# Kernel tuning notes

Measured on AMD Instinct MI355X. Metric: run time of the kernel, lower is better.

Reference implementation:

```python
import jax, jax.numpy as jnp
import numpy as np

R = 3          # radius
T_STEPS = 2    # T
F = 200        # fingerprint_dim
AOUT = 39
BOUT = 10
B, L, N, NB = 128, 256, 8, 512


def _gru(x, h, wih, whh, bih, bhh):
    # PyTorch GRUCell semantics; wih/whh: [3F, F], gate order r,z,n
    gi = x @ wih.T + bih
    gh = h @ whh.T + bhh
    ir, iz, inn = jnp.split(gi, 3, axis=-1)
    hr, hz, hn = jnp.split(gh, 3, axis=-1)
    r = jax.nn.sigmoid(ir + hr)
    z = jax.nn.sigmoid(iz + hz)
    n = jnp.tanh(inn + r * hn)
    return (1.0 - z) * n + z * h


def _seg_softmax(x, lo, hi):
    idx = jnp.arange(x.shape[-1])
    m = ((idx >= lo) & (idx < hi)).astype(x.dtype)
    s = jax.nn.softmax(x + (1.0 - m) * (-9e8), axis=-1)
    return s * m


def _unit_act(x, i, fn):
    m = (jnp.arange(x.shape[-1]) == i).astype(x.dtype)
    return fn(x * m) * m


def setup_inputs() -> dict:
    key = jax.random.key(0)
    ks = jax.random.split(key, 24)
    rn = lambda k, s, sc=0.05: (jax.random.normal(k, s, jnp.float32) * sc)
    inp = {
        'atom_list': rn(ks[0], (B, L, AOUT), 1.0),
        'bond_list': rn(ks[1], (B, NB, BOUT), 1.0),
        'atom_degree_list': jax.random.randint(ks[2], (B, L, N), 0, L),
        'bond_degree_list': jax.random.randint(ks[3], (B, L, N), 0, NB),
        'atom_mask': jnp.ones((B, L), jnp.float32),
        'mol_feature': rn(ks[4], (B, F), 1.0),
        'activated_features': jax.nn.relu(rn(ks[5], (B, L, F), 1.0)),
        # params
        'atom_fc_w': rn(ks[6], (AOUT, F)), 'atom_fc_b': jnp.zeros((AOUT,), jnp.float32),
        'bond_fc_w': rn(ks[7], (BOUT, 2 * F)), 'bond_fc_b': jnp.zeros((BOUT,), jnp.float32),
        'align_w': rn(ks[8], (R, F, 2 * F)), 'align_b': jnp.zeros((R, F), jnp.float32),
        'attend_w': rn(ks[9], (R, F, F)), 'attend_b': jnp.zeros((R, F), jnp.float32),
        'gru_wih': rn(ks[10], (R, 3 * F, F)), 'gru_whh': rn(ks[11], (R, 3 * F, F)),
        'gru_bih': jnp.zeros((R, 3 * F), jnp.float32), 'gru_bhh': jnp.zeros((R, 3 * F), jnp.float32),
        'mol_align_w': rn(ks[12], (F, 2 * F)), 'mol_align_b': jnp.zeros((F,), jnp.float32),
        'mol_gru_wih': rn(ks[13], (3 * F, F)), 'mol_gru_whh': rn(ks[14], (3 * F, F)),
        'mol_gru_bih': jnp.zeros((3 * F,), jnp.float32), 'mol_gru_bhh': jnp.zeros((3 * F,), jnp.float32),
    }
    return inp


def reference(atom_list, bond_list, atom_degree_list, bond_degree_list, atom_mask,
              mol_feature, activated_features,
              atom_fc_w, atom_fc_b, bond_fc_w, bond_fc_b,
              align_w, align_b, attend_w, attend_b,
              gru_wih, gru_whh, gru_bih, gru_bhh,
              mol_align_w, mol_align_b,
              mol_gru_wih, mol_gru_whh, mol_gru_bih, mol_gru_bhh):
    f32 = jnp.float32
    b, l, _ = atom_list.shape
    fdim = mol_feature.shape[-1]
    gather = jax.vmap(lambda feats, idx: feats[idx])  # [L,F],[L,N] -> [L,N,F]

    pad = (atom_degree_list == l - 1)
    attend_mask = jnp.where(pad, 0.0, 1.0).astype(f32)[..., None]      # [B,L,N,1]
    softmax_mask = jnp.where(pad, -9e8, 0.0).astype(f32)[..., None]    # [B,L,N,1]

    # molecular feature -> per-atom git feature (T GRU steps)
    mol_exp = jnp.broadcast_to(mol_feature[:, None, :], (b, l, fdim))
    mw = jax.nn.softmax(jnp.sum(mol_exp * activated_features, axis=-1), axis=-1)  # [B,L]
    git = mw[..., None] * mol_exp + activated_features
    for _t in range(T_STEPS):
        ctx = jax.nn.elu(jnp.concatenate([mol_exp, git], axis=-1) @ mol_align_w.T + mol_align_b)
        git = _gru(ctx.reshape(b * l, fdim), git.reshape(b * l, fdim),
                   mol_gru_wih, mol_gru_whh, mol_gru_bih, mol_gru_bhh).reshape(b, l, fdim)
        act = jax.nn.relu(git)

    # radius-1 rounds of neighbor attention + GRU update
    for d in range(R - 1):
        nbr = gather(act, atom_degree_list)                             # [B,L,N,F]
        exp = jnp.broadcast_to(act[:, :, None, :], nbr.shape)
        feat_align = jnp.concatenate([exp, nbr], axis=-1)               # [B,L,N,2F]
        score = jax.nn.leaky_relu(feat_align @ align_w[d].T + align_b[d], 0.01)
        score = score + softmax_mask
        attw = jax.nn.softmax(score, axis=-2) * attend_mask             # [B,L,N,F]
        nt = nbr @ attend_w[d].T + attend_b[d]
        context = jax.nn.elu(jnp.sum(attw * nt, axis=-2))               # [B,L,F]
        h = _gru(context.reshape(b * l, fdim), act.reshape(b * l, fdim),
                 gru_wih[d], gru_whh[d], gru_bih[d], gru_bhh[d])
        act = jax.nn.relu(h.reshape(b, l, fdim))

    # decode atoms and bonds
    al = act @ atom_fc_w.T + atom_fc_b                                  # [B,L,AOUT]
    nbr = gather(act, atom_degree_list)                                 # [B,L,N,F]
    exp = jnp.broadcast_to(act[:, :, None, :], nbr.shape)
    bl = jnp.concatenate([exp, nbr], axis=-1) @ bond_fc_w.T + bond_fc_b  # [B,L,N,BOUT]

    sig = jax.nn.sigmoid
    activate_atom = (_seg_softmax(al, 0, 16) + _seg_softmax(al, 16, 22)
                     + _seg_softmax(al, 24, 30) + _seg_softmax(al, 31, 36)
                     + _unit_act(al, 24, jax.nn.relu)
                     + _unit_act(al, 30, sig) + _unit_act(al, 36, sig)
                     + _unit_act(al, 37, sig) + _unit_act(al, 38, sig))
    activate_bond = (_seg_softmax(bl, 0, 4) + _seg_softmax(bl, 6, 10)
                     + _unit_act(bl, 4, sig) + _unit_act(bl, 5, sig))
    return (activate_atom, activate_bond)
```

## Files before the change

### kernel.cpp

```cpp
#include <hip/hip_runtime.h>
#include <hip/hip_bf16.h>

#define FDIM 200
#define BB   128
#define LL   256
#define NN   8
#define BL   (BB*LL)
#define AOUTD 39
#define BOUTD 10
#define KCH  28

#define P0 0
#define P1 17920
#define P2 25088
#define P3 46592
#define P4 82432
#define P5 103936
#define P6 139776
#define P7 161280
#define WCHUNKS 164864
#define NBIAS 4864

typedef short v8s __attribute__((ext_vector_type(8)));
typedef float v4f __attribute__((ext_vector_type(4)));

__device__ __forceinline__ float bf2f(unsigned short u){
  union { unsigned int i; float f; } v; v.i = ((unsigned int)u) << 16; return v.f;
}
__device__ __forceinline__ unsigned short f2bf(float f){
  unsigned int x = __float_as_uint(f);
  x += 0x7fffu + ((x >> 16) & 1u);
  return (unsigned short)(x >> 16);
}
__device__ __forceinline__ float ldf(const void* p, long long i, bool bf){
  return bf ? bf2f(((const unsigned short*)p)[i]) : ((const float*)p)[i];
}
__device__ __forceinline__ void stf(void* p, size_t i, float v, bool bf){
  if (bf) ((unsigned short*)p)[i] = f2bf(v);
  else    ((float*)p)[i] = v;
}
__device__ __forceinline__ float bflo(unsigned int q){
  union { unsigned int i; float f; } v; v.i = q << 16; return v.f;
}
__device__ __forceinline__ float bfhi(unsigned int q){
  union { unsigned int i; float f; } v; v.i = q & 0xffff0000u; return v.f;
}
__device__ __forceinline__ void ld8(const unsigned short* p, float* o){
  uint4 q = *(const uint4*)p;
  o[0]=bflo(q.x); o[1]=bfhi(q.x); o[2]=bflo(q.y); o[3]=bfhi(q.y);
  o[4]=bflo(q.z); o[5]=bfhi(q.z); o[6]=bflo(q.w); o[7]=bfhi(q.w);
}
__device__ __forceinline__ void ld8g(const void* p, size_t i, bool bf, float* o){
  if (bf){ ld8((const unsigned short*)p + i, o); }
  else {
    const float4* q = (const float4*)((const float*)p + i);
    float4 x = q[0], y = q[1];
    o[0]=x.x; o[1]=x.y; o[2]=x.z; o[3]=x.w;
    o[4]=y.x; o[5]=y.y; o[6]=y.z; o[7]=y.w;
  }
}
__device__ __forceinline__ void st8(unsigned short* p, const float* v){
  uint4 q;
  q.x = (unsigned int)f2bf(v[0]) | ((unsigned int)f2bf(v[1]) << 16);
  q.y = (unsigned int)f2bf(v[2]) | ((unsigned int)f2bf(v[3]) << 16);
  q.z = (unsigned int)f2bf(v[4]) | ((unsigned int)f2bf(v[5]) << 16);
  q.w = (unsigned int)f2bf(v[6]) | ((unsigned int)f2bf(v[7]) << 16);
  *(uint4*)p = q;
}
__device__ __forceinline__ float dotF(const void* wp, size_t off, const float* x, bool bf){
  float a0=0.f,a1=0.f,a2=0.f,a3=0.f;
  if (bf){
    const uint4* p = (const uint4*)((const unsigned short*)wp + off);
#pragma unroll
    for (int c = 0; c < FDIM/8; ++c){
      uint4 q = p[c];
      const float* xb = x + c*8;
      a0 += bflo(q.x)*xb[0]; a1 += bfhi(q.x)*xb[1];
      a2 += bflo(q.y)*xb[2]; a3 += bfhi(q.y)*xb[3];
      a0 += bflo(q.z)*xb[4]; a1 += bfhi(q.z)*xb[5];
      a2 += bflo(q.w)*xb[6]; a3 += bfhi(q.w)*xb[7];
    }
  } else {
    const float4* p = (const float4*)((const float*)wp + off);
#pragma unroll
    for (int c = 0; c < FDIM/4; ++c){
      float4 q = p[c];
      const float* xb = x + c*4;
      a0 += q.x*xb[0]; a1 += q.y*xb[1]; a2 += q.z*xb[2]; a3 += q.w*xb[3];
    }
  }
  return (a0+a1)+(a2+a3);
}
__device__ __forceinline__ float sigm(float x){ return 1.f/(1.f+__expf(-x)); }
__device__ __forceinline__ float tanh_(float x){
  float cx = fminf(fmaxf(x, -15.f), 15.f);
  float e = __expf(2.f*cx);
  return (e - 1.f)/(e + 1.f);
}
__device__ __forceinline__ float elu_(float x){ return x > 0.f ? x : __expf(x) - 1.f; }

__global__ void k_probe(const unsigned int* __restrict__ amask, int* __restrict__ mode){
  if (blockIdx.x == 0 && threadIdx.x == 0)
    *mode = (amask[0] == 0x3F803F80u) ? 1 : 0;
}

__global__ __launch_bounds__(256) void k_repack(unsigned short* __restrict__ wrep,
    const void* mwhh, const void* maw, const void* mwih,
    const void* alw, const void* atw, const void* gwhh, const void* gwih,
    const void* afw, const void* bfw, const int* __restrict__ mode){
  const bool bf = (*mode != 0);
  int idx = blockIdx.x*256 + threadIdx.x;
  if (idx >= WCHUNKS) return;
  int pb, Ng, pad = 0; long long d = 0;
  if (idx < P1)      { pb = P0; Ng = 640;  }
  else if (idx < P2) { pb = P1; Ng = 256;  }
  else if (idx < P3) { pb = P2; Ng = 768;  pad = 1; }
  else if (idx < P4) { pb = P3; Ng = 1280; }
  else if (idx < P5) { pb = P4; Ng = 768;  pad = 1; }
  else if (idx < P6) { pb = P5; Ng = 1280; d = 1; }
  else if (idx < P7) { pb = P6; Ng = 768;  pad = 1; d = 1; }
  else               { pb = P7; Ng = 128;  }
  int li = idx - pb;
  int c = li / Ng, n = li - c*Ng;
  const void* S = nullptr; long long sb = 0; int rl = 0, off = 0, row = 0, N = 0;
  if (pad){
    int gate = n >> 8, f = n & 255;
    if (f < 200){
      S = (pb == P2) ? mwih : gwih;
      sb = (pb == P2) ? 0 : d*120000;
      rl = 200; off = 0; row = gate*200 + f; N = Ng;
    }
  }
  else if (pb == P0)      { S = mwhh; rl = 200; row = n; N = 600; }
  else if (pb == P1) { S = maw;  rl = 400; off = 200; row = n; N = 200; }
  else if (pb == P3 || pb == P5){
    N = 1200;
    if (n < 200)      { S = alw;  sb = d*80000;  rl = 400; off = 0;   row = n; }
    else if (n < 400) { S = alw;  sb = d*80000;  rl = 400; off = 200; row = n-200; }
    else if (n < 600) { S = atw;  sb = d*40000;  rl = 200; off = 0;   row = n-400; }
    else              { S = gwhh; sb = d*120000; rl = 200; off = 0;   row = n-600; }
  } else {
    N = 64;
    if (n < 39)                { S = afw; rl = 200; row = n; }
    else if (n >= 40 && n < 50){ S = bfw; rl = 400; off = 0;   row = n-40; }
    else if (n >= 50 && n < 60){ S = bfw; rl = 400; off = 200; row = n-50; }
  }
  float v[8];
#pragma unroll
  for (int j = 0; j < 8; j++){
    int k = c*8 + j;
    v[j] = (S && n < N && k < 200) ? ldf(S, sb + (long long)row*rl + off + k, bf) : 0.f;
  }
  st8(wrep + (size_t)idx*8, v);
}

__global__ __launch_bounds__(256) void k_biases(float* __restrict__ bt,
    const void* mbhh, const void* mbih, const void* alb, const void* atb,
    const void* gbhh, const void* gbih, const void* afb, const void* bfb,
    const int* __restrict__ mode){
  const bool bf = (*mode != 0);
  int e = blockIdx.x*256 + threadIdx.x;
  if (e >= NBIAS) return;
  float v = 0.f;
  if (e < 600)        v = ldf(mbhh, e, bf);
  else if (e < 1200)  v = ldf(mbih, e-600, bf);
  else if (e < 4800){
    int q = e - 1200; int d = q / 1800; q -= d*1800;
    if (q < 1200){
      if (q < 200)      v = ldf(alb, (long long)d*200 + q, bf);
      else if (q < 400) v = 0.f;
      else if (q < 600) v = ldf(atb, (long long)d*200 + q-400, bf);
      else              v = ldf(gbhh, (long long)d*600 + q-600, bf);
    } else              v = ldf(gbih, (long long)d*600 + q-1200, bf);
  } else {
    int q = e - 4800;
    if (q < 39)                 v = ldf(afb, q, bf);
    else if (q >= 40 && q < 50) v = ldf(bfb, q-40, bf);
  }
  bt[e] = v;
}

__global__ __launch_bounds__(256, 5) void k_gemm(
    const unsigned short* __restrict__ A,
    const unsigned short* __restrict__ Wc, int wNg, int npan,
    unsigned short* __restrict__ C, int ldc, int Nout,
    int emode, const float* __restrict__ bias, int gbase)
{
  __shared__ unsigned short Ws[KCH*64*8];
  int t = threadIdx.x;
  int bid = blockIdx.x;
  int res = bid & 7, q = bid >> 3;
  int p = q % npan;
  int mt = (q / npan)*8 + res;
  int nbase = p * 64;
  int mbase = mt * 128;
  const uint4* Wg = (const uint4*)Wc;
  uint4* Wl = (uint4*)Ws;
  for (int i = t; i < KCH*64; i += 256){
    int c = i >> 6, n = i & 63;
    Wl[i] = Wg[(size_t)c*wNg + nbase + n];
  }
  __syncthreads();
  int wave = t >> 6, lane = t & 63;
  int quad = lane >> 4, l16 = lane & 15;
  const unsigned short* A0 = A + (size_t)(mbase + wave*32 + l16)*FDIM + quad*8;
  v4f acc[2][4];
#pragma unroll
  for (int ms = 0; ms < 2; ms++)
#pragma unroll
    for (int ns = 0; ns < 4; ns++) acc[ms][ns] = (v4f){0.f,0.f,0.f,0.f};
#pragma unroll
  for (int ks = 0; ks < 7; ks++){
    v8s a0 = *(const v8s*)(A0 + ks*32);
    v8s a1 = *(const v8s*)(A0 + 16*FDIM + ks*32);
    const unsigned short* Bp = Ws + ((ks*4 + quad)*64 + l16)*8;
#pragma unroll
    for (int ns = 0; ns < 4; ns++){
      v8s b = *(const v8s*)(Bp + ns*128);
      acc[0][ns] = __builtin_amdgcn_mfma_f32_16x16x32_bf16(a0, b, acc[0][ns], 0, 0, 0);
      acc[1][ns] = __builtin_amdgcn_mfma_f32_16x16x32_bf16(a1, b, acc[1][ns], 0, 0, 0);
    }
  }
  __syncthreads();
  const float* pr = (emode == 2) ? (bias + (size_t)(((gbase + mbase) >> 8))*FDIM) : nullptr;
#pragma unroll
  for (int ms = 0; ms < 2; ms++){
#pragma unroll
    for (int ns = 0; ns < 4; ns++){
      int lcol = l16 + ns*16;
      int col = nbase + lcol;
      float badd = (emode == 1) ? bias[col] : 0.f;
      float pv   = (emode == 2) ? pr[col] : 0.f;
      int lrow = wave*32 + ms*16 + quad*4;
#pragma unroll
      for (int reg = 0; reg < 4; reg++){
        float v = acc[ms][ns][reg] + badd;
        if (emode == 2) v = elu_(pv + v);
        Ws[(lrow + reg)*72 + lcol] = f2bf(v);
      }
    }
  }
  __syncthreads();
#pragma unroll
  for (int j = 0; j < 4; j++){
    int g = t + j*256;
    int row = g >> 3, cg = g & 7;
    int col = nbase + cg*8;
    if (col < Nout){
      uint4 qv = *(const uint4*)(Ws + row*72 + cg*8);
      *(uint4*)(C + (size_t)(mbase + row)*ldc + col) = qv;
    }
  }
}

__global__ __launch_bounds__(256, 3) void k_gemm_gru(
    const unsigned short* __restrict__ ctxA,
    const unsigned short* __restrict__ Wc,
    unsigned short* __restrict__ act,
    const unsigned short* __restrict__ big, int gho,
    const float* __restrict__ gib, int dorelu)
{
  __shared__ unsigned short Ws[3*KCH*32*8];
  int t = threadIdx.x, bid = blockIdx.x;
  int res = bid & 7, q = bid >> 3;
  int p = q % 7;
  int mt = (q / 7)*8 + res;
  int f0 = p*32;
  int mbase = mt*128;
  const uint4* Wg = (const uint4*)Wc;
  uint4* Wl = (uint4*)Ws;
  for (int i = t; i < 3*KCH*32; i += 256){
    int g = i / (KCH*32), r2 = i - g*(KCH*32);
    int c = r2 >> 5, n = r2 & 31;
    Wl[i] = Wg[(size_t)c*768 + g*256 + f0 + n];
  }
  __syncthreads();
  int wave = t >> 6, lane = t & 63;
  int quad = lane >> 4, l16 = lane & 15;
  const unsigned short* A0 = ctxA + (size_t)(mbase + wave*32 + l16)*FDIM + quad*8;
  v4f acc[3][2][2];
#pragma unroll
  for (int g = 0; g < 3; g++)
#pragma unroll
    for (int ms = 0; ms < 2; ms++)
#pragma unroll
      for (int ns = 0; ns < 2; ns++) acc[g][ms][ns] = (v4f){0.f,0.f,0.f,0.f};
#pragma unroll
  for (int ks = 0; ks < 7; ks++){
    v8s a0 = *(const v8s*)(A0 + ks*32);
    v8s a1 = *(const v8s*)(A0 + 16*FDIM + ks*32);
#pragma unroll
    for (int g = 0; g < 3; g++){
      const unsigned short* Bp = Ws + ((size_t)(g*KCH + ks*4 + quad)*32 + l16)*8;
#pragma unroll
      for (int ns = 0; ns < 2; ns++){
        v8s b = *(const v8s*)(Bp + ns*128);
        acc[g][0][ns] = __builtin_amdgcn_mfma_f32_16x16x32_bf16(a0, b, acc[g][0][ns], 0, 0, 0);
        acc[g][1][ns] = __builtin_amdgcn_mfma_f32_16x16x32_bf16(a1, b, acc[g][1][ns], 0, 0, 0);
      }
    }
  }
  int rowb = mbase + wave*32 + quad*4;
#pragma unroll
  for (int ms = 0; ms < 2; ms++){
#pragma unroll
    for (int ns = 0; ns < 2; ns++){
      int f = f0 + ns*16 + l16;
      if (f < 200){
        float br = gib[f], bz = gib[200+f], bn = gib[400+f];
#pragma unroll
        for (int reg = 0; reg < 4; reg++){
          int row = rowb + ms*16 + reg;
          size_t gb = (size_t)row*1200 + gho;
          float ghr = bf2f(big[gb + f]);
          float ghz = bf2f(big[gb + 200 + f]);
          float ghn = bf2f(big[gb + 400 + f]);
          float h = bf2f(act[(size_t)row*FDIM + f]);
          float r = sigm(acc[0][ms][ns][reg] + br + ghr);
          float z = sigm(acc[1][ms][ns][reg] + bz + ghz);
          float n = tanh_(acc[2][ms][ns][reg] + bn + r*ghn);
          float hn = (1.f - z)*n + z*h;
          if (dorelu) hn = fmaxf(hn, 0.f);
          act[(size_t)row*FDIM + f] = f2bf(hn);
        }
      }
    }
  }
}

__global__ __launch_bounds__(256) void k_premol(float* __restrict__ pre,
    const void* __restrict__ molf, const void* __restrict__ maw,
    const void* __restrict__ mab, const int* __restrict__ mode){
  const bool bf = (*mode != 0);
  int b = blockIdx.x, t = threadIdx.x;
  __shared__ float mf[FDIM];
  for (int f = t; f < FDIM; f += 256) mf[f] = ldf(molf, (size_t)b*FDIM+f, bf);
  __syncthreads();
  for (int f = t; f < FDIM; f += 256)
    pre[b*FDIM+f] = ldf(mab, f, bf) + dotF(maw, (size_t)f*2*FDIM, mf, bf);
}

__global__ __launch_bounds__(LL) void k_gitdot(float* __restrict__ mw_out,
    const void* __restrict__ molf, const void* __restrict__ actf,
    const int* __restrict__ mode){
  const bool bf = (*mode != 0);
  int b = blockIdx.x, l = threadIdx.x;
  __shared__ float mf[FDIM];
  __shared__ float red[LL];
  for (int f = l; f < FDIM; f += LL) mf[f] = ldf(molf, (size_t)b*FDIM+f, bf);
  __syncthreads();
  float d = dotF(actf, ((size_t)b*LL + l)*FDIM, mf, bf);
  red[l] = d; __syncthreads();
  for (int s = 128; s > 0; s >>= 1){ if (l < s) red[l] = fmaxf(red[l], red[l+s]); __syncthreads(); }
  float m = red[0]; __syncthreads();
  float e = __expf(d - m);
  red[l] = e; __syncthreads();
  for (int s = 128; s > 0; s >>= 1){ if (l < s) red[l] += red[l+s]; __syncthreads(); }
  mw_out[(size_t)b*LL + l] = e / red[0];
}

__global__ __launch_bounds__(256) void k_gitwrite(unsigned short* __restrict__ act,
    const void* __restrict__ molf, const void* __restrict__ actf,
    const float* __restrict__ mw, const int* __restrict__ mode){
  const bool bf = (*mode != 0);
  int idx = blockIdx.x*256 + threadIdx.x;
  if (idx >= BL*25) return;
  int row = idx/25, f0 = (idx - row*25)*8;
  int b = row >> 8;
  float m = mw[row];
  float mv[8], av[8], v[8];
  ld8g(molf, (size_t)b*FDIM + f0, bf, mv);
  ld8g(actf, (size_t)row*FDIM + f0, bf, av);
#pragma unroll
  for (int j = 0; j < 8; j++) v[j] = m*mv[j] + av[j];
  st8(act + (size_t)row*FDIM + f0, v);
}

__global__ __launch_bounds__(256) void k_attn_ew(const unsigned short* __restrict__ big,
    unsigned short* __restrict__ ctx, const int* __restrict__ adeg,
    int base, int total){
  int idx = blockIdx.x*256 + threadIdx.x;
  if (idx >= total) return;
  int a = idx/25, f0 = (idx - a*25)*8;
  int mb = (a >> 8) << 8;
  float s0[8];
  ld8(big + (size_t)a*1200 + f0, s0);
  int4 d0 = *(const int4*)(adeg + (size_t)(base + a)*NN);
  int4 d1 = *(const int4*)(adeg + (size_t)(base + a)*NN + 4);
  int iv[NN] = {d0.x, d0.y, d0.z, d0.w, d1.x, d1.y, d1.z, d1.w};
  int nid[NN]; float nmul[NN], nadd[NN];
#pragma unroll
  for (int n = 0; n < NN; n++){
    nid[n] = mb + iv[n];
    bool pad = (iv[n] == LL-1);
    nmul[n] = pad ? 0.f : 1.f;
    nadd[n] = pad ? -9e8f : 0.f;
  }
  float e[NN][8], mx[8];
#pragma unroll
  for (int j = 0; j < 8; j++) mx[j] = -1e30f;
#pragma unroll
  for (int n = 0; n < NN; n++){
    float p[8];
    ld8(big + (size_t)nid[n]*1200 + 200 + f0, p);
#pragma unroll
    for (int j = 0; j < 8; j++){
      float s = s0[j] + p[j];
      s = s > 0.f ? s : 0.01f*s;
      s += nadd[n];
      e[n][j] = s;
      mx[j] = fmaxf(mx[j], s);
    }
  }
  float sum[8] = {0,0,0,0,0,0,0,0};
#pragma unroll
  for (int n = 0; n < NN; n++)
#pragma unroll
    for (int j = 0; j < 8; j++){ e[n][j] = __expf(e[n][j] - mx[j]); sum[j] += e[n][j]; }
  float acc[8] = {0,0,0,0,0,0,0,0};
#pragma unroll
  for (int n = 0; n < NN; n++){
    float q[8];
    ld8(big + (size_t)nid[n]*1200 + 400 + f0, q);
#pragma unroll
    for (int j = 0; j < 8; j++) acc[j] += e[n][j]*nmul[n]*q[j];
  }
  float o[8];
#pragma unroll
  for (int j = 0; j < 8; j++) o[j] = elu_(acc[j]/sum[j]);
  st8(ctx + (size_t)a*FDIM + f0, o);
}

__global__ __launch_bounds__(256) void k_dec(const unsigned short* __restrict__ big,
    const int* __restrict__ adeg, void* __restrict__ out, int base,
    const int* __restrict__ mode){
  const bool bf = (*mode != 0);
  const size_t obase = (size_t)BL*AOUTD;
  int sub = threadIdx.x >> 6, tl = threadIdx.x & 63;
  int a = blockIdx.x*4 + sub;
  __shared__ float al[4][40];
  __shared__ float sm[4][4], ss[4][4];
  const int lo[4] = {0,16,24,31}, hi[4] = {16,22,30,36};
  if (tl < AOUTD) al[sub][tl] = bf2f(big[(size_t)a*64 + tl]);
  __syncthreads();
  if (tl < 4){
    float m = -1e30f;
    for (int k = lo[tl]; k < hi[tl]; k++) m = fmaxf(m, al[sub][k]);
    float s = 0.f;
    for (int k = lo[tl]; k < hi[tl]; k++) s += __expf(al[sub][k]-m);
    sm[sub][tl] = m; ss[sub][tl] = s;
  }
  __syncthreads();
  if (tl < AOUTD){
    float v = 0.f;
#pragma unroll
    for (int g = 0; g < 4; g++)
      if (tl >= lo[g] && tl < hi[g]) v += __expf(al[sub][tl]-sm[sub][g])/ss[sub][g];
    if (tl == 24) v += fmaxf(al[sub][24], 0.f);
    if (tl == 30 || tl == 36 || tl == 37 || tl == 38) v += sigm(al[sub][tl]);
    stf(out, (size_t)(base + a)*AOUTD + tl, v, bf);
  } else if (tl >= 40 && tl < 48){
    int n = tl - 40;
    int iv = adeg[((size_t)(base + a))*NN + n];
    int vr = ((a >> 8) << 8) + iv;
    float bl[BOUTD];
#pragma unroll
    for (int o = 0; o < BOUTD; o++)
      bl[o] = bf2f(big[(size_t)a*64 + 40 + o]) + bf2f(big[(size_t)vr*64 + 50 + o]);
    float v[BOUTD];
    float m0 = fmaxf(fmaxf(bl[0],bl[1]), fmaxf(bl[2],bl[3]));
    float e0[4], s0 = 0.f;
#pragma unroll
    for (int j = 0; j < 4; j++){ e0[j] = __expf(bl[j]-m0); s0 += e0[j]; }
    float m1 = fmaxf(fmaxf(bl[6],bl[7]), fmaxf(bl[8],bl[9]));
    float e1[4], s1 = 0.f;
#pragma unroll
    for (int j = 0; j < 4; j++){ e1[j] = __expf(bl[6+j]-m1); s1 += e1[j]; }
#pragma unroll
    for (int j = 0; j < 4; j++) v[j] = e0[j]/s0;
    v[4] = sigm(bl[4]); v[5] = sigm(bl[5]);
#pragma unroll
    for (int j = 0; j < 4; j++) v[6+j] = e1[j]/s1;
    size_t op = obase + ((size_t)(base + a)*NN + n)*BOUTD;
#pragma unroll
    for (int j = 0; j < BOUTD; j++) stf(out, op + j, v[j], bf);
  }
}

extern "C" void kernel_launch(void* const* d_in, const int* in_sizes, int n_in,
                              void* d_out, int out_size, void* d_ws, size_t ws_size,
                              hipStream_t stream) {
  const int* adeg = (const int*)d_in[2];
  const void* amask = d_in[4];
  const void* molf = d_in[5];
  const void* actf = d_in[6];
  const void* afw = d_in[7];  const void* afb = d_in[8];
  const void* bfw = d_in[9];  const void* bfb = d_in[10];
  const void* alw = d_in[11]; const void* alb = d_in[12];
  const void* atw = d_in[13]; const void* atb = d_in[14];
  const void* gwih = d_in[15]; const void* gwhh = d_in[16];
  const void* gbih = d_in[17]; const void* gbhh = d_in[18];
  const void* maw = d_in[19]; const void* mab = d_in[20];
  const void* mwih = d_in[21]; const void* mwhh = d_in[22];
  const void* mbih = d_in[23]; const void* mbhh = d_in[24];

  char* w = (char*)d_ws;
  unsigned short* act  = (unsigned short*)w;  w += (size_t)BL*FDIM*2;
  float*          mw   = (float*)w;           w += (size_t)BL*4;
  float*          pre  = (float*)w;           w += (size_t)BB*FDIM*4;
  unsigned short* wrep = (unsigned short*)w;  w += (size_t)WCHUNKS*16;
  float*          bt   = (float*)w;           w += (size_t)NBIAS*4;
  int*            mode = (int*)w;             w += 16;
  size_t fixed = (size_t)(w - (char*)d_ws);
  int CH = 8192;
  if (ws_size >= fixed + (size_t)32768*2800) CH = 32768;
  else if (ws_size >= fixed + (size_t)16384*2800) CH = 16384;
  unsigned short* ctx = (unsigned short*)w;   w += (size_t)CH*FDIM*2;
  unsigned short* big = (unsigned short*)w;
  const int NCH = BL / CH;
  const int EWT = CH*25, EWB = EWT/256;
  const int GY = CH/128;

  k_probe<<<1, 64, 0, stream>>>((const unsigned int*)amask, mode);
  k_repack<<<(WCHUNKS + 255)/256, 256, 0, stream>>>(wrep, mwhh, maw, mwih,
      alw, atw, gwhh, gwih, afw, bfw, mode);
  k_biases<<<(NBIAS + 255)/256, 256, 0, stream>>>(bt, mbhh, mbih, alb, atb,
      gbhh, gbih, afb, bfb, mode);
  k_premol<<<BB, 256, 0, stream>>>(pre, molf, maw, mab, mode);
  k_gitdot<<<BB, LL, 0, stream>>>(mw, molf, actf, mode);
  k_gitwrite<<<(BL*25 + 255)/256, 256, 0, stream>>>(act, molf, actf, mw, mode);

  for (int ts = 0; ts < 2; ts++){
    for (int c = 0; c < NCH; c++){
      int base = c*CH;
      unsigned short* Ac = act + (size_t)base*FDIM;
      k_gemm<<<10*GY, 256, 0, stream>>>(Ac, wrep + (size_t)P0*8, 640, 10,
          big, 1200, 600, 1, bt + 0, 0);
      k_gemm<<<4*GY, 256, 0, stream>>>(Ac, wrep + (size_t)P1*8, 256, 4,
          ctx, FDIM, FDIM, 2, pre, base);
      k_gemm_gru<<<7*GY, 256, 0, stream>>>(ctx, wrep + (size_t)P2*8,
          Ac, big, 0, bt + 600, (ts==1));
    }
  }
  for (int d = 0; d < 2; d++){
    size_t pA = (d ? P5 : P3), pB = (d ? P6 : P4);
    float* btA = bt + 1200 + d*1800;
    float* gib = bt + 2400 + d*1800;
    for (int c = 0; c < NCH; c++){
      int base = c*CH;
      unsigned short* Ac = act + (size_t)base*FDIM;
      k_gemm<<<19*GY, 256, 0, stream>>>(Ac, wrep + pA*8, 1280, 19,
          big, 1200, 1200, 1, btA, 0);
      k_attn_ew<<<EWB, 256, 0, stream>>>(big, ctx, adeg, base, EWT);
      k_gemm_gru<<<7*GY, 256, 0, stream>>>(ctx, wrep + pB*8,
          Ac, big, 600, gib, 1);
    }
  }
  for (int c = 0; c < NCH; c++){
    int base = c*CH;
    unsigned short* Ac = act + (size_t)base*FDIM;
    k_gemm<<<1*GY, 256, 0, stream>>>(Ac, wrep + (size_t)P7*8, 128, 1,
        big, 64, 64, 1, bt + 4800, 0);
    k_dec<<<CH/4, 256, 0, stream>>>(big, adeg, d_out, base, mode);
  }
}
```

Measured before the change: 549.8 us.

## Fuse hidden-state GRU GEMM into GRU kernel with ping-pong activation buffers

The h@Whh GEMM that was computed by a separate k_gemm pass and stored as bf16 in the 'big' buffer now runs inside the GRU kernel, which computes both input and hidden gate products (six slots) and applies the gate math in registers. Activations are double-buffered (act0/act1) so the fused kernel can read the old state while writing the new one without a hazard. This removes the intermediate gh write and read, shrinks the attention GEMM output width, and allows larger chunks for the same workspace. In exchange the GRU kernel has twice the accumulators, a narrower 16-column tile and more blocks, and it adds an extra full activation buffer.

```diff
diff --git a/kernel.cpp b/kernel.cpp
--- a/kernel.cpp
+++ b/kernel.cpp
@@ -10,15 +10,14 @@
 #define BOUTD 10
 #define KCH  28
 
-#define P0 0
-#define P1 17920
-#define P2 25088
-#define P3 46592
-#define P4 82432
-#define P5 103936
-#define P6 139776
-#define P7 161280
-#define WCHUNKS 164864
+#define P1C 0
+#define PMG 7168
+#define PA0 50176
+#define PG0 68096
+#define PA1 111104
+#define PG1 129024
+#define PD  172032
+#define WCHUNKS 175616
 #define NBIAS 4864
 
 typedef short v8s __attribute__((ext_vector_type(8)));
@@ -105,42 +104,38 @@
 }
 
 __global__ __launch_bounds__(256) void k_repack(unsigned short* __restrict__ wrep,
-    const void* mwhh, const void* maw, const void* mwih,
-    const void* alw, const void* atw, const void* gwhh, const void* gwih,
+    const void* maw, const void* mwih, const void* mwhh,
+    const void* alw, const void* atw, const void* gwih, const void* gwhh,
     const void* afw, const void* bfw, const int* __restrict__ mode){
   const bool bf = (*mode != 0);
   int idx = blockIdx.x*256 + threadIdx.x;
   if (idx >= WCHUNKS) return;
-  int pb, Ng, pad = 0; long long d = 0;
-  if (idx < P1)      { pb = P0; Ng = 640;  }
-  else if (idx < P2) { pb = P1; Ng = 256;  }
-  else if (idx < P3) { pb = P2; Ng = 768;  pad = 1; }
-  else if (idx < P4) { pb = P3; Ng = 1280; }
-  else if (idx < P5) { pb = P4; Ng = 768;  pad = 1; }
-  else if (idx < P6) { pb = P5; Ng = 1280; d = 1; }
-  else if (idx < P7) { pb = P6; Ng = 768;  pad = 1; d = 1; }
-  else               { pb = P7; Ng = 128;  }
+  int pb, Ng, kind; long long d = 0;
+  if (idx < PMG)      { pb = P1C; Ng = 256;  kind = 0; }
+  else if (idx < PA0) { pb = PMG; Ng = 1536; kind = 1; }
+  else if (idx < PG0) { pb = PA0; Ng = 640;  kind = 2; d = 0; }
+  else if (idx < PA1) { pb = PG0; Ng = 1536; kind = 3; d = 0; }
+  else if (idx < PG1) { pb = PA1; Ng = 640;  kind = 2; d = 1; }
+  else if (idx < PD)  { pb = PG1; Ng = 1536; kind = 3; d = 1; }
+  else                { pb = PD;  Ng = 128;  kind = 4; }
   int li = idx - pb;
   int c = li / Ng, n = li - c*Ng;
-  const void* S = nullptr; long long sb = 0; int rl = 0, off = 0, row = 0, N = 0;
-  if (pad){
-    int gate = n >> 8, f = n & 255;
+  const void* S = nullptr; long long sb = 0; int rl = 0, off = 0, row = 0;
+  if (kind == 0){ if (n < 200){ S = maw; rl = 400; off = 200; row = n; } }
+  else if (kind == 1 || kind == 3){
+    int slot = n >> 8, f = n & 255;
     if (f < 200){
-      S = (pb == P2) ? mwih : gwih;
-      sb = (pb == P2) ? 0 : d*120000;
-      rl = 200; off = 0; row = gate*200 + f; N = Ng;
-    }
-  }
-  else if (pb == P0)      { S = mwhh; rl = 200; row = n; N = 600; }
-  else if (pb == P1) { S = maw;  rl = 400; off = 200; row = n; N = 200; }
-  else if (pb == P3 || pb == P5){
-    N = 1200;
-    if (n < 200)      { S = alw;  sb = d*80000;  rl = 400; off = 0;   row = n; }
-    else if (n < 400) { S = alw;  sb = d*80000;  rl = 400; off = 200; row = n-200; }
-    else if (n < 600) { S = atw;  sb = d*40000;  rl = 200; off = 0;   row = n-400; }
-    else              { S = gwhh; sb = d*120000; rl = 200; off = 0;   row = n-600; }
+      int gate = (slot < 3) ? slot : slot - 3;
+      if (kind == 1) S = (slot < 3) ? mwih : mwhh;
+      else         { S = (slot < 3) ? gwih : gwhh; sb = d*120000; }
+      rl = 200; row = gate*200 + f;
+    }
+  }
+  else if (kind == 2){
+    if (n < 200)      { S = alw; sb = d*80000; rl = 400; off = 0;   row = n; }
+    else if (n < 400) { S = alw; sb = d*80000; rl = 400; off = 200; row = n-200; }
+    else if (n < 600) { S = atw; sb = d*40000; rl = 200; off = 0;   row = n-400; }
   } else {
-    N = 64;
     if (n < 39)                { S = afw; rl = 200; row = n; }
     else if (n >= 40 && n < 50){ S = bfw; rl = 400; off = 0;   row = n-40; }
     else if (n >= 50 && n < 60){ S = bfw; rl = 400; off = 200; row = n-50; }
@@ -149,7 +144,7 @@
 #pragma unroll
   for (int j = 0; j < 8; j++){
     int k = c*8 + j;
-    v[j] = (S && n < N && k < 200) ? ldf(S, sb + (long long)row*rl + off + k, bf) : 0.f;
+    v[j] = (S && k < 200) ? ldf(S, sb + (long long)row*rl + off + k, bf) : 0.f;
   }
   st8(wrep + (size_t)idx*8, v);
 }
@@ -229,7 +224,7 @@
     for (int ns = 0; ns < 4; ns++){
       int lcol = l16 + ns*16;
       int col = nbase + lcol;
-      float badd = (emode == 1) ? bias[col] : 0.f;
+      float badd = (emode == 1 && col < Nout) ? bias[col] : 0.f;
       float pv   = (emode == 2) ? pr[col] : 0.f;
       int lrow = wave*32 + ms*16 + quad*4;
 #pragma unroll
@@ -253,76 +248,69 @@
   }
 }
 
-__global__ __launch_bounds__(256, 3) void k_gemm_gru(
+__global__ __launch_bounds__(256, 3) void k_gru2(
     const unsigned short* __restrict__ ctxA,
+    const unsigned short* __restrict__ actS,
+    unsigned short* __restrict__ actD,
     const unsigned short* __restrict__ Wc,
-    unsigned short* __restrict__ act,
-    const unsigned short* __restrict__ big, int gho,
-    const float* __restrict__ gib, int dorelu)
+    const float* __restrict__ gib, const float* __restrict__ ghb,
+    int dorelu)
 {
-  __shared__ unsigned short Ws[3*KCH*32*8];
+  __shared__ unsigned short Ws[6*KCH*16*8];
   int t = threadIdx.x, bid = blockIdx.x;
   int res = bid & 7, q = bid >> 3;
-  int p = q % 7;
-  int mt = (q / 7)*8 + res;
-  int f0 = p*32;
+  int p = q % 13;
+  int mt = (q / 13)*8 + res;
+  int f0 = p*16;
   int mbase = mt*128;
   const uint4* Wg = (const uint4*)Wc;
   uint4* Wl = (uint4*)Ws;
-  for (int i = t; i < 3*KCH*32; i += 256){
-    int g = i / (KCH*32), r2 = i - g*(KCH*32);
-    int c = r2 >> 5, n = r2 & 31;
-    Wl[i] = Wg[(size_t)c*768 + g*256 + f0 + n];
+  for (int i = t; i < 6*KCH*16; i += 256){
+    int s = i / (KCH*16), r2 = i - s*(KCH*16);
+    int c = r2 >> 4, n = r2 & 15;
+    Wl[i] = Wg[(size_t)c*1536 + s*256 + f0 + n];
   }
   __syncthreads();
   int wave = t >> 6, lane = t & 63;
   int quad = lane >> 4, l16 = lane & 15;
-  const unsigned short* A0 = ctxA + (size_t)(mbase + wave*32 + l16)*FDIM + quad*8;
-  v4f acc[3][2][2];
-#pragma unroll
-  for (int g = 0; g < 3; g++)
-#pragma unroll
-    for (int ms = 0; ms < 2; ms++)
-#pragma unroll
-      for (int ns = 0; ns < 2; ns++) acc[g][ms][ns] = (v4f){0.f,0.f,0.f,0.f};
+  const unsigned short* Ac = ctxA + (size_t)(mbase + wave*32 + l16)*FDIM + quad*8;
+  const unsigned short* Ah = actS + (size_t)(mbase + wave*32 + l16)*FDIM + quad*8;
+  v4f acc[6][2];
+#pragma unroll
+  for (int s = 0; s < 6; s++)
+#pragma unroll
+    for (int ms = 0; ms < 2; ms++) acc[s][ms] = (v4f){0.f,0.f,0.f,0.f};
 #pragma unroll
   for (int ks = 0; ks < 7; ks++){
-    v8s a0 = *(const v8s*)(A0 + ks*32);
-    v8s a1 = *(const v8s*)(A0 + 16*FDIM + ks*32);
-#pragma unroll
-    for (int g = 0; g < 3; g++){
-      const unsigned short* Bp = Ws + ((size_t)(g*KCH + ks*4 + quad)*32 + l16)*8;
-#pragma unroll
-      for (int ns = 0; ns < 2; ns++){
-        v8s b = *(const v8s*)(Bp + ns*128);
-        acc[g][0][ns] = __builtin_amdgcn_mfma_f32_16x16x32_bf16(a0, b, acc[g][0][ns], 0, 0, 0);
-        acc[g][1][ns] = __builtin_amdgcn_mfma_f32_16x16x32_bf16(a1, b, acc[g][1][ns], 0, 0, 0);
-      }
-    }
-  }
-  int rowb = mbase + wave*32 + quad*4;
-#pragma unroll
-  for (int ms = 0; ms < 2; ms++){
-#pragma unroll
-    for (int ns = 0; ns < 2; ns++){
-      int f = f0 + ns*16 + l16;
-      if (f < 200){
-        float br = gib[f], bz = gib[200+f], bn = gib[400+f];
-#pragma unroll
-        for (int reg = 0; reg < 4; reg++){
-          int row = rowb + ms*16 + reg;
-          size_t gb = (size_t)row*1200 + gho;
-          float ghr = bf2f(big[gb + f]);
-          float ghz = bf2f(big[gb + 200 + f]);
-          float ghn = bf2f(big[gb + 400 + f]);
-          float h = bf2f(act[(size_t)row*FDIM + f]);
-          float r = sigm(acc[0][ms][ns][reg] + br + ghr);
-          float z = sigm(acc[1][ms][ns][reg] + bz + ghz);
-          float n = tanh_(acc[2][ms][ns][reg] + bn + r*ghn);
-          float hn = (1.f - z)*n + z*h;
-          if (dorelu) hn = fmaxf(hn, 0.f);
-          act[(size_t)row*FDIM + f] = f2bf(hn);
-        }
+    v8s c0 = *(const v8s*)(Ac + ks*32);
+    v8s c1 = *(const v8s*)(Ac + 16*FDIM + ks*32);
+    v8s h0 = *(const v8s*)(Ah + ks*32);
+    v8s h1 = *(const v8s*)(Ah + 16*FDIM + ks*32);
+#pragma unroll
+    for (int s = 0; s < 6; s++){
+      v8s b = *(const v8s*)(Ws + ((size_t)(s*KCH + ks*4 + quad)*16 + l16)*8);
+      v8s x0 = (s < 3) ? c0 : h0;
+      v8s x1 = (s < 3) ? c1 : h1;
+      acc[s][0] = __builtin_amdgcn_mfma_f32_16x16x32_bf16(x0, b, acc[s][0], 0, 0, 0);
+      acc[s][1] = __builtin_amdgcn_mfma_f32_16x16x32_bf16(x1, b, acc[s][1], 0, 0, 0);
+    }
+  }
+  int f = f0 + l16;
+  if (f < 200){
+    float bir = gib[f], biz = gib[200+f], bin = gib[400+f];
+    float bhr = ghb[f], bhz = ghb[200+f], bhn = ghb[400+f];
+#pragma unroll
+    for (int ms = 0; ms < 2; ms++){
+#pragma unroll
+      for (int reg = 0; reg < 4; reg++){
+        int row = mbase + wave*32 + ms*16 + quad*4 + reg;
+        float h = bf2f(actS[(size_t)row*FDIM + f]);
+        float r = sigm(acc[0][ms][reg] + bir + acc[3][ms][reg] + bhr);
+        float z = sigm(acc[1][ms][reg] + biz + acc[4][ms][reg] + bhz);
+        float n = tanh_(acc[2][ms][reg] + bin + r*(acc[5][ms][reg] + bhn));
+        float hn = (1.f - z)*n + z*h;
+        if (dorelu) hn = fmaxf(hn, 0.f);
+        actD[(size_t)row*FDIM + f] = f2bf(hn);
       }
     }
   }
@@ -384,7 +372,7 @@
   int a = idx/25, f0 = (idx - a*25)*8;
   int mb = (a >> 8) << 8;
   float s0[8];
-  ld8(big + (size_t)a*1200 + f0, s0);
+  ld8(big + (size_t)a*600 + f0, s0);
   int4 d0 = *(const int4*)(adeg + (size_t)(base + a)*NN);
   int4 d1 = *(const int4*)(adeg + (size_t)(base + a)*NN + 4);
   int iv[NN] = {d0.x, d0.y, d0.z, d0.w, d1.x, d1.y, d1.z, d1.w};
@@ -402,7 +390,7 @@
 #pragma unroll
   for (int n = 0; n < NN; n++){
     float p[8];
-    ld8(big + (size_t)nid[n]*1200 + 200 + f0, p);
+    ld8(big + (size_t)nid[n]*600 + 200 + f0, p);
 #pragma unroll
     for (int j = 0; j < 8; j++){
       float s = s0[j] + p[j];
@@ -421,7 +409,7 @@
 #pragma unroll
   for (int n = 0; n < NN; n++){
     float q[8];
-    ld8(big + (size_t)nid[n]*1200 + 400 + f0, q);
+    ld8(big + (size_t)nid[n]*600 + 400 + f0, q);
 #pragma unroll
     for (int j = 0; j < 8; j++) acc[j] += e[n][j]*nmul[n]*q[j];
   }
@@ -505,7 +493,8 @@
   const void* mbih = d_in[23]; const void* mbhh = d_in[24];
 
   char* w = (char*)d_ws;
-  unsigned short* act  = (unsigned short*)w;  w += (size_t)BL*FDIM*2;
+  unsigned short* act0 = (unsigned short*)w;  w += (size_t)BL*FDIM*2;
+  unsigned short* act1 = (unsigned short*)w;  w += (size_t)BL*FDIM*2;
   float*          mw   = (float*)w;           w += (size_t)BL*4;
   float*          pre  = (float*)w;           w += (size_t)BB*FDIM*4;
   unsigned short* wrep = (unsigned short*)w;  w += (size_t)WCHUNKS*16;
@@ -513,8 +502,8 @@
   int*            mode = (int*)w;             w += 16;
   size_t fixed = (size_t)(w - (char*)d_ws);
   int CH = 8192;
-  if (ws_size >= fixed + (size_t)32768*2800) CH = 32768;
-  else if (ws_size >= fixed + (size_t)16384*2800) CH = 16384;
+  if (ws_size >= fixed + (size_t)32768*1600) CH = 32768;
+  else if (ws_size >= fixed + (size_t)16384*1600) CH = 16384;
   unsigned short* ctx = (unsigned short*)w;   w += (size_t)CH*FDIM*2;
   unsigned short* big = (unsigned short*)w;
   const int NCH = BL / CH;
@@ -522,44 +511,48 @@
   const int GY = CH/128;
 
   k_probe<<<1, 64, 0, stream>>>((const unsigned int*)amask, mode);
-  k_repack<<<(WCHUNKS + 255)/256, 256, 0, stream>>>(wrep, mwhh, maw, mwih,
-      alw, atw, gwhh, gwih, afw, bfw, mode);
+  k_repack<<<(WCHUNKS + 255)/256, 256, 0, stream>>>(wrep, maw, mwih, mwhh,
+      alw, atw, gwih, gwhh, afw, bfw, mode);
   k_biases<<<(NBIAS + 255)/256, 256, 0, stream>>>(bt, mbhh, mbih, alb, atb,
       gbhh, gbih, afb, bfb, mode);
   k_premol<<<BB, 256, 0, stream>>>(pre, molf, maw, mab, mode);
   k_gitdot<<<BB, LL, 0, stream>>>(mw, molf, actf, mode);
-  k_gitwrite<<<(BL*25 + 255)/256, 256, 0, stream>>>(act, molf, actf, mw, mode);
+  k_gitwrite<<<(BL*25 + 255)/256, 256, 0, stream>>>(act0, molf, actf, mw, mode);
+
+  unsigned short* cur = act0;
+  unsigned short* alt = act1;
 
   for (int ts = 0; ts < 2; ts++){
     for (int c = 0; c < NCH; c++){
       int base = c*CH;
-      unsigned short* Ac = act + (size_t)base*FDIM;
-      k_gemm<<<10*GY, 256, 0, stream>>>(Ac, wrep + (size_t)P0*8, 640, 10,
-          big, 1200, 600, 1, bt + 0, 0);
-      k_gemm<<<4*GY, 256, 0, stream>>>(Ac, wrep + (size_t)P1*8, 256, 4,
+      unsigned short* Ac = cur + (size_t)base*FDIM;
+      k_gemm<<<4*GY, 256, 0, stream>>>(Ac, wrep + (size_t)P1C*8, 256, 4,
           ctx, FDIM, FDIM, 2, pre, base);
-      k_gemm_gru<<<7*GY, 256, 0, stream>>>(ctx, wrep + (size_t)P2*8,
-          Ac, big, 0, bt + 600, (ts==1));
-    }
+      k_gru2<<<13*GY, 256, 0, stream>>>(ctx, Ac, alt + (size_t)base*FDIM,
+          wrep + (size_t)PMG*8, bt + 600, bt + 0, (ts==1));
+    }
+    { unsigned short* tmp = cur; cur = alt; alt = tmp; }
   }
   for (int d = 0; d < 2; d++){
-    size_t pA = (d ? P5 : P3), pB = (d ? P6 : P4);
+    size_t pA = (d ? PA1 : PA0), pG = (d ? PG1 : PG0);
     float* btA = bt + 1200 + d*1800;
     float* gib = bt + 2400 + d*1800;
+    float* ghb = bt + 1800 + d*1800;
     for (int c = 0; c < NCH; c++){
       int base = c*CH;
-      unsigned short* Ac = act + (size_t)base*FDIM;
-      k_gemm<<<19*GY, 256, 0, stream>>>(Ac, wrep + pA*8, 1280, 19,
-          big, 1200, 1200, 1, btA, 0);
+      unsigned short* Ac = cur + (size_t)base*FDIM;
+      k_gemm<<<10*GY, 256, 0, stream>>>(Ac, wrep + pA*8, 640, 10,
+          big, 600, 600, 1, btA, 0);
       k_attn_ew<<<EWB, 256, 0, stream>>>(big, ctx, adeg, base, EWT);
-      k_gemm_gru<<<7*GY, 256, 0, stream>>>(ctx, wrep + pB*8,
-          Ac, big, 600, gib, 1);
-    }
+      k_gru2<<<13*GY, 256, 0, stream>>>(ctx, Ac, alt + (size_t)base*FDIM,
+          wrep + pG*8, gib, ghb, 1);
+    }
+    { unsigned short* tmp = cur; cur = alt; alt = tmp; }
   }
   for (int c = 0; c < NCH; c++){
     int base = c*CH;
-    unsigned short* Ac = act + (size_t)base*FDIM;
-    k_gemm<<<1*GY, 256, 0, stream>>>(Ac, wrep + (size_t)P7*8, 128, 1,
+    unsigned short* Ac = cur + (size_t)base*FDIM;
+    k_gemm<<<1*GY, 256, 0, stream>>>(Ac, wrep + (size_t)PD*8, 128, 1,
         big, 64, 64, 1, bt + 4800, 0);
     k_dec<<<CH/4, 256, 0, stream>>>(big, adeg, d_out, base, mode);
   }
```

Result: faster. 529.3 us (median of 2 runs) (-3.7%).
